# Performance work log

Measured on AMD Instinct MI355X. Metric: run time of the kernel, lower is better.

## Reference

```python
import jax, jax.numpy as jnp
import numpy as np

B, CIN, H, W = 16, 32, 256, 256
COUT, KH, KW = 32, 3, 3
NUM_EXPERTS = 8
PAD = ((1, 1), (1, 1))  # static 'same' padding for 3x3, stride 1, dilation 1


def setup_inputs() -> dict:
    key = jax.random.key(0)
    k_x, k_r, k_w, k_b = jax.random.split(key, 4)
    x = jax.random.normal(k_x, (B, CIN, H, W), dtype=jnp.float32)
    # routing weights are typically sigmoid/softmax outputs in [0,1]
    routing_weights = jax.nn.softmax(jax.random.normal(k_r, (B, NUM_EXPERTS), dtype=jnp.float32), axis=-1)
    num_params = COUT * CIN * KH * KW  # groups=1 -> in_channels//groups = CIN
    expert_weight = jax.random.normal(k_w, (NUM_EXPERTS, num_params), dtype=jnp.float32) * 0.05
    expert_bias = jax.random.normal(k_b, (NUM_EXPERTS, COUT), dtype=jnp.float32) * 0.05
    return {"x": x, "routing_weights": routing_weights,
            "expert_weight": expert_weight, "expert_bias": expert_bias}


def reference(x, routing_weights, expert_weight, expert_bias):
    b = x.shape[0]
    # Per-sample kernels: [B, num_params] -> [B, COUT, CIN, KH, KW]
    w = jnp.matmul(routing_weights, expert_weight).reshape(b, COUT, CIN, KH, KW)
    bias = jnp.matmul(routing_weights, expert_bias)  # [B, COUT]

    def conv_one(xi, wi):
        # xi: [CIN, H, W], wi: [COUT, CIN, KH, KW]
        return jax.lax.conv_general_dilated(
            xi[None], wi, window_strides=(1, 1), padding=PAD,
            dimension_numbers=("NCHW", "OIHW", "NCHW"))[0]

    out = jax.vmap(conv_one)(x, w)  # [B, COUT, H, W]
    out = out + bias[:, :, None, None]
    return out
```

## Files before the change

kernel.cpp:

```cpp
#include <hip/hip_runtime.h>

#define B_   16
#define CIN  32
#define COUT 32
#define HH   256
#define WW   256
#define NE   8
#define NTAP 9
#define KTOT (NTAP * CIN)

#define TH 8
#define TW 32
#define LROWS (TH + 2)
#define LCOLS (TW + 2)
#define PXS   40
#define NI    ((TW + 8) / 4)

typedef __attribute__((ext_vector_type(8))) short  short8;
typedef __attribute__((ext_vector_type(4))) float  floatx4;

__device__ __forceinline__ unsigned short f2bf(float f) {
    unsigned int u = __float_as_uint(f);
    u += 0x7FFFu + ((u >> 16) & 1u);
    return (unsigned short)(u >> 16);
}

__global__ __launch_bounds__(256) void prep_weights(
    const float* __restrict__ routing,
    const float* __restrict__ ew,
    const float* __restrict__ eb,
    unsigned short* __restrict__ ws_w,
    float* __restrict__ ws_b)
{
    const int b = blockIdx.x;
    const int t = threadIdx.x;
    float r[NE];
#pragma unroll
    for (int e = 0; e < NE; ++e) r[e] = routing[b * NE + e];

    for (int idx = t; idx < COUT * KTOT; idx += 256) {
        const int co  = idx / KTOT;
        const int k   = idx - co * KTOT;
        const int tap = k >> 5;
        const int ci  = k & 31;
        float acc = 0.f;
#pragma unroll
        for (int e = 0; e < NE; ++e)
            acc += r[e] * ew[e * (COUT * CIN * 9) + co * (CIN * 9) + ci * 9 + tap];
        ws_w[(b * COUT + co) * KTOT + k] = f2bf(acc);
    }
    if (t < COUT) {
        float acc = 0.f;
#pragma unroll
        for (int e = 0; e < NE; ++e) acc += r[e] * eb[e * COUT + t];
        ws_b[b * COUT + t] = acc;
    }
}

__global__ __launch_bounds__(256, 5) void condconv_mfma(
    const float* __restrict__ x,
    const unsigned short* __restrict__ wsw,
    const float* __restrict__ wsb,
    float* __restrict__ out)
{
    __shared__ __align__(16) unsigned short s_x[LROWS * LCOLS * PXS];

    const int b    = blockIdx.z;
    const int x0   = blockIdx.x * TW;
    const int y0   = blockIdx.y * TH;
    const int t    = threadIdx.x;
    const int lane = t & 63;
    const int wv   = t >> 6;
    const int ln   = lane & 15;
    const int quad = lane >> 4;

    for (int task = t; task < LROWS * NI * 4; task += 256) {
        const int cg  = task & 3;
        const int ri  = task >> 2;
        const int i   = ri % NI;
        const int row = ri / NI;
        const int gy  = y0 + row - 1;
        const int gx  = x0 + 4 * i - 4;
        floatx4 v[8];
        if (gy >= 0 && gy < HH && gx >= 0 && gx < WW) {
            const float* src = x + (((size_t)b * CIN + cg * 8) * HH + gy) * WW + gx;
#pragma unroll
            for (int u = 0; u < 8; ++u)
                v[u] = *(const floatx4*)(src + (size_t)u * HH * WW);
        } else {
#pragma unroll
            for (int u = 0; u < 8; ++u) v[u] = (floatx4){0.f, 0.f, 0.f, 0.f};
        }
#pragma unroll
        for (int j = 0; j < 4; ++j) {
            const int lcol = 4 * i + j - 3;
            if (lcol >= 0 && lcol < LCOLS) {
                short8 pk;
#pragma unroll
                for (int u = 0; u < 8; ++u) pk[u] = (short)f2bf(v[u][j]);
                *(short8*)&s_x[(row * LCOLS + lcol) * PXS + cg * 8] = pk;
            }
        }
    }

    const unsigned short* wb = wsw + (size_t)b * COUT * KTOT;
    short8 wfc0 = *(const short8*)(wb + ln * KTOT + quad * 8);
    short8 wfc1 = *(const short8*)(wb + (16 + ln) * KTOT + quad * 8);

    floatx4 acc[4][2];
#pragma unroll
    for (int tt = 0; tt < 4; ++tt)
#pragma unroll
        for (int h = 0; h < 2; ++h)
            acc[tt][h] = (floatx4){0.f, 0.f, 0.f, 0.f};

    int base[4];
#pragma unroll
    for (int tt = 0; tt < 4; ++tt)
        base[tt] = ((2 * wv + (tt >> 1)) * LCOLS + (tt & 1) * 16 + ln) * PXS + quad * 8;

    __syncthreads();

#pragma unroll 1
    for (int tap = 0; tap < NTAP; ++tap) {
        const int tn = (tap < NTAP - 1) ? tap + 1 : NTAP - 1;
        const short8 wfn0 = *(const short8*)(wb + ln * KTOT + tn * 32 + quad * 8);
        const short8 wfn1 = *(const short8*)(wb + (16 + ln) * KTOT + tn * 32 + quad * 8);
        const int dy  = tap / 3;
        const int dx  = tap - dy * 3;
        const int off = (dy * LCOLS + dx) * PXS;
#pragma unroll
        for (int tt = 0; tt < 4; ++tt) {
            const short8 pfr = *(const short8*)&s_x[base[tt] + off];
            acc[tt][0] = __builtin_amdgcn_mfma_f32_16x16x32_bf16(pfr, wfc0, acc[tt][0], 0, 0, 0);
            acc[tt][1] = __builtin_amdgcn_mfma_f32_16x16x32_bf16(pfr, wfc1, acc[tt][1], 0, 0, 0);
        }
        wfc0 = wfn0;
        wfc1 = wfn1;
    }

    float bias_v[2];
    bias_v[0] = wsb[b * COUT + ln];
    bias_v[1] = wsb[b * COUT + 16 + ln];

#pragma unroll
    for (int tt = 0; tt < 4; ++tt) {
        const int gy = y0 + 2 * wv + (tt >> 1);
        const int gx = x0 + (tt & 1) * 16 + quad * 4;
#pragma unroll
        for (int h = 0; h < 2; ++h) {
            floatx4 vo = acc[tt][h];
#pragma unroll
            for (int e = 0; e < 4; ++e) vo[e] += bias_v[h];
            const int co = h * 16 + ln;
            *(floatx4*)(out + (((size_t)b * COUT + co) * HH + gy) * WW + gx) = vo;
        }
    }
}

extern "C" void kernel_launch(void* const* d_in, const int* in_sizes, int n_in,
                              void* d_out, int out_size, void* d_ws, size_t ws_size,
                              hipStream_t stream) {
    const float* x       = (const float*)d_in[0];
    const float* routing = (const float*)d_in[1];
    const float* ew      = (const float*)d_in[2];
    const float* eb      = (const float*)d_in[3];
    float* out = (float*)d_out;

    unsigned short* ws_w = (unsigned short*)d_ws;
    float* ws_b = (float*)((char*)d_ws + (size_t)B_ * COUT * KTOT * 2);

    prep_weights<<<dim3(B_), dim3(256), 0, stream>>>(routing, ew, eb, ws_w, ws_b);

    dim3 grid(WW / TW, HH / TH, B_);
    condconv_mfma<<<grid, dim3(256), 0, stream>>>(x, ws_w, ws_b, out);
}
```

Baseline: 289.0 us.

## Stream row chunks through LDS ring buffer with register-prefetched next rows

Each block now walks 8 consecutive 8-row tiles down the image. Input rows sit in a 16-row LDS ring buffer, so the 2-row halo is reused between steps instead of being reloaded. The next 8 rows are loaded into registers while the current tile's MFMAs run. All 9 tap weight fragments and the bias are also loaded into registers once per block. The cost is more registers, fewer resident blocks (launch bounds drop from 5 to 2), fewer blocks in the grid, and two barriers per step.

```diff
diff --git a/kernel.cpp b/kernel.cpp
--- a/kernel.cpp
+++ b/kernel.cpp
@@ -9,12 +9,15 @@
 #define NTAP 9
 #define KTOT (NTAP * CIN)
 
+#define TW 32
 #define TH 8
-#define TW 32
-#define LROWS (TH + 2)
+#define NSTEP 8
+#define CHROWS (TH * NSTEP)
 #define LCOLS (TW + 2)
 #define PXS   40
-#define NI    ((TW + 8) / 4)
+#define ROWU  1536
+#define NRING 16
+#define NI    10
 
 typedef __attribute__((ext_vector_type(8))) short  short8;
 typedef __attribute__((ext_vector_type(4))) float  floatx4;
@@ -57,29 +60,39 @@
     }
 }
 
-__global__ __launch_bounds__(256, 5) void condconv_mfma(
+__global__ __launch_bounds__(256, 2) void condconv_mfma(
     const float* __restrict__ x,
     const unsigned short* __restrict__ wsw,
     const float* __restrict__ wsb,
     float* __restrict__ out)
 {
-    __shared__ __align__(16) unsigned short s_x[LROWS * LCOLS * PXS];
+    __shared__ __align__(16) unsigned short s_x[NRING * ROWU];
 
     const int b    = blockIdx.z;
     const int x0   = blockIdx.x * TW;
-    const int y0   = blockIdx.y * TH;
+    const int ych  = blockIdx.y * CHROWS;
     const int t    = threadIdx.x;
     const int lane = t & 63;
     const int wv   = t >> 6;
     const int ln   = lane & 15;
     const int quad = lane >> 4;
 
-    for (int task = t; task < LROWS * NI * 4; task += 256) {
+    const unsigned short* wb = wsw + (size_t)b * COUT * KTOT;
+    short8 wf0[NTAP], wf1[NTAP];
+#pragma unroll
+    for (int tap = 0; tap < NTAP; ++tap) {
+        wf0[tap] = *(const short8*)(wb + ln * KTOT + tap * 32 + quad * 8);
+        wf1[tap] = *(const short8*)(wb + (16 + ln) * KTOT + tap * 32 + quad * 8);
+    }
+    const float bias0 = wsb[b * COUT + ln];
+    const float bias1 = wsb[b * COUT + 16 + ln];
+
+    for (int task = t; task < 10 * NI * 4; task += 256) {
         const int cg  = task & 3;
         const int ri  = task >> 2;
         const int i   = ri % NI;
         const int row = ri / NI;
-        const int gy  = y0 + row - 1;
+        const int gy  = ych - 1 + row;
         const int gx  = x0 + 4 * i - 4;
         floatx4 v[8];
         if (gy >= 0 && gy < HH && gx >= 0 && gx < WW) {
@@ -91,6 +104,7 @@
 #pragma unroll
             for (int u = 0; u < 8; ++u) v[u] = (floatx4){0.f, 0.f, 0.f, 0.f};
         }
+        const int slot = (gy + 1) & (NRING - 1);
 #pragma unroll
         for (int j = 0; j < 4; ++j) {
             const int lcol = 4 * i + j - 3;
@@ -98,62 +112,128 @@
                 short8 pk;
 #pragma unroll
                 for (int u = 0; u < 8; ++u) pk[u] = (short)f2bf(v[u][j]);
-                *(short8*)&s_x[(row * LCOLS + lcol) * PXS + cg * 8] = pk;
-            }
-        }
-    }
-
-    const unsigned short* wb = wsw + (size_t)b * COUT * KTOT;
-    short8 wfc0 = *(const short8*)(wb + ln * KTOT + quad * 8);
-    short8 wfc1 = *(const short8*)(wb + (16 + ln) * KTOT + quad * 8);
-
-    floatx4 acc[4][2];
+                *(short8*)&s_x[slot * ROWU + lcol * PXS + cg * 8] = pk;
+            }
+        }
+    }
+
+    const int cg0  = t & 3;
+    const int ri0  = t >> 2;
+    const int i0   = ri0 % NI;
+    const int rn0  = ri0 / NI;
+    const int gx0  = x0 + 4 * i0 - 4;
+    const bool xok0 = (gx0 >= 0 && gx0 < WW);
+    const int ri1  = 64 + ri0;
+    const int i1   = ri1 % NI;
+    const int rn1  = ri1 / NI;
+    const int gx1  = x0 + 4 * i1 - 4;
+    const bool xok1 = (gx1 >= 0 && gx1 < WW);
+
+    int cpart[4];
 #pragma unroll
     for (int tt = 0; tt < 4; ++tt)
-#pragma unroll
-        for (int h = 0; h < 2; ++h)
-            acc[tt][h] = (floatx4){0.f, 0.f, 0.f, 0.f};
-
-    int base[4];
-#pragma unroll
-    for (int tt = 0; tt < 4; ++tt)
-        base[tt] = ((2 * wv + (tt >> 1)) * LCOLS + (tt & 1) * 16 + ln) * PXS + quad * 8;
+        cpart[tt] = ((tt & 1) * 16 + ln) * PXS + quad * 8;
+
+    int rb   = ych & (NRING - 1);
+    int swr0 = (ych + 10 + rn0) & (NRING - 1);
+    int swr1 = (ych + 10 + rn1) & (NRING - 1);
 
     __syncthreads();
 
 #pragma unroll 1
-    for (int tap = 0; tap < NTAP; ++tap) {
-        const int tn = (tap < NTAP - 1) ? tap + 1 : NTAP - 1;
-        const short8 wfn0 = *(const short8*)(wb + ln * KTOT + tn * 32 + quad * 8);
-        const short8 wfn1 = *(const short8*)(wb + (16 + ln) * KTOT + tn * 32 + quad * 8);
-        const int dy  = tap / 3;
-        const int dx  = tap - dy * 3;
-        const int off = (dy * LCOLS + dx) * PXS;
+    for (int k = 0; k < NSTEP; ++k) {
+        const int y0k  = ych + 8 * k;
+        const bool last = (k == NSTEP - 1);
+
+        floatx4 v0[8], v1[8];
+        if (!last) {
+            const int gyn0 = y0k + 9 + rn0;
+            if (xok0 && gyn0 < HH) {
+                const float* s0 = x + (((size_t)b * CIN + cg0 * 8) * HH + gyn0) * WW + gx0;
+#pragma unroll
+                for (int u = 0; u < 8; ++u)
+                    v0[u] = *(const floatx4*)(s0 + (size_t)u * HH * WW);
+            } else {
+#pragma unroll
+                for (int u = 0; u < 8; ++u) v0[u] = (floatx4){0.f, 0.f, 0.f, 0.f};
+            }
+            if (wv == 0) {
+                const int gyn1 = y0k + 9 + rn1;
+                if (xok1 && gyn1 < HH) {
+                    const float* s1 = x + (((size_t)b * CIN + cg0 * 8) * HH + gyn1) * WW + gx1;
+#pragma unroll
+                    for (int u = 0; u < 8; ++u)
+                        v1[u] = *(const floatx4*)(s1 + (size_t)u * HH * WW);
+                } else {
+#pragma unroll
+                    for (int u = 0; u < 8; ++u) v1[u] = (floatx4){0.f, 0.f, 0.f, 0.f};
+                }
+            }
+        }
+        __builtin_amdgcn_sched_barrier(0);
+
+        floatx4 acc[4][2];
 #pragma unroll
         for (int tt = 0; tt < 4; ++tt) {
-            const short8 pfr = *(const short8*)&s_x[base[tt] + off];
-            acc[tt][0] = __builtin_amdgcn_mfma_f32_16x16x32_bf16(pfr, wfc0, acc[tt][0], 0, 0, 0);
-            acc[tt][1] = __builtin_amdgcn_mfma_f32_16x16x32_bf16(pfr, wfc1, acc[tt][1], 0, 0, 0);
-        }
-        wfc0 = wfn0;
-        wfc1 = wfn1;
-    }
-
-    float bias_v[2];
-    bias_v[0] = wsb[b * COUT + ln];
-    bias_v[1] = wsb[b * COUT + 16 + ln];
-
-#pragma unroll
-    for (int tt = 0; tt < 4; ++tt) {
-        const int gy = y0 + 2 * wv + (tt >> 1);
-        const int gx = x0 + (tt & 1) * 16 + quad * 4;
-#pragma unroll
-        for (int h = 0; h < 2; ++h) {
-            floatx4 vo = acc[tt][h];
-#pragma unroll
-            for (int e = 0; e < 4; ++e) vo[e] += bias_v[h];
-            const int co = h * 16 + ln;
-            *(floatx4*)(out + (((size_t)b * COUT + co) * HH + gy) * WW + gx) = vo;
+            acc[tt][0] = (floatx4){0.f, 0.f, 0.f, 0.f};
+            acc[tt][1] = (floatx4){0.f, 0.f, 0.f, 0.f};
+        }
+#pragma unroll
+        for (int tap = 0; tap < NTAP; ++tap) {
+            const int dy = tap / 3;
+            const int dx = tap - dy * 3;
+            int so[2];
+#pragma unroll
+            for (int rg = 0; rg < 2; ++rg)
+                so[rg] = ((rb + 2 * wv + rg + dy) & (NRING - 1)) * ROWU + dx * PXS;
+#pragma unroll
+            for (int tt = 0; tt < 4; ++tt) {
+                const short8 pfr = *(const short8*)&s_x[so[tt >> 1] + cpart[tt]];
+                acc[tt][0] = __builtin_amdgcn_mfma_f32_16x16x32_bf16(pfr, wf0[tap], acc[tt][0], 0, 0, 0);
+                acc[tt][1] = __builtin_amdgcn_mfma_f32_16x16x32_bf16(pfr, wf1[tap], acc[tt][1], 0, 0, 0);
+            }
+        }
+
+#pragma unroll
+        for (int tt = 0; tt < 4; ++tt) {
+            const int gy = y0k + 2 * wv + (tt >> 1);
+            const int gx = x0 + (tt & 1) * 16 + quad * 4;
+            floatx4 o0 = acc[tt][0];
+            floatx4 o1 = acc[tt][1];
+#pragma unroll
+            for (int e = 0; e < 4; ++e) { o0[e] += bias0; o1[e] += bias1; }
+            *(floatx4*)(out + (((size_t)b * COUT + ln)      * HH + gy) * WW + gx) = o0;
+            *(floatx4*)(out + (((size_t)b * COUT + 16 + ln) * HH + gy) * WW + gx) = o1;
+        }
+
+        if (!last) {
+            __syncthreads();
+#pragma unroll
+            for (int j = 0; j < 4; ++j) {
+                const int lcol = 4 * i0 + j - 3;
+                if (lcol >= 0 && lcol < LCOLS) {
+                    short8 pk;
+#pragma unroll
+                    for (int u = 0; u < 8; ++u) pk[u] = (short)f2bf(v0[u][j]);
+                    *(short8*)&s_x[swr0 * ROWU + lcol * PXS + cg0 * 8] = pk;
+                }
+            }
+            if (wv == 0) {
+#pragma unroll
+                for (int j = 0; j < 4; ++j) {
+                    const int lcol = 4 * i1 + j - 3;
+                    if (lcol >= 0 && lcol < LCOLS) {
+                        short8 pk;
+#pragma unroll
+                        for (int u = 0; u < 8; ++u) pk[u] = (short)f2bf(v1[u][j]);
+                        *(short8*)&s_x[swr1 * ROWU + lcol * PXS + cg0 * 8] = pk;
+                    }
+                }
+            }
+            __syncthreads();
+            rb   = (rb + 8)   & (NRING - 1);
+            swr0 = (swr0 + 8) & (NRING - 1);
+            swr1 = (swr1 + 8) & (NRING - 1);
         }
     }
 }
@@ -172,6 +252,6 @@
 
     prep_weights<<<dim3(B_), dim3(256), 0, stream>>>(routing, ew, eb, ws_w, ws_b);
 
-    dim3 grid(WW / TW, HH / TH, B_);
+    dim3 grid(WW / TW, HH / CHROWS, B_);
     condconv_mfma<<<grid, dim3(256), 0, stream>>>(x, ws_w, ws_b, out);
 }
```

Result: slower. 296.2 us (+2.5%).

## Stream full-width row chunks through an LDS ring buffer with register-resident weights

Applied to the files above, without the earlier changes.

Replaces the small 8x32 tiles with blocks that each own a full-width strip of 16 rows. Each block keeps a 6-slot ring of bf16 input rows in LDS and prefetches the next two rows into registers while MFMAs run on the current pair. All nine tap weight fragments are loaded into registers once per block. This removes halo re-reads between neighbouring tiles and the per-tap weight loads. The cost is far fewer blocks (256 of 512 threads), higher register and LDS pressure, and two barriers per step.

```diff
diff --git a/kernel.cpp b/kernel.cpp
--- a/kernel.cpp
+++ b/kernel.cpp
@@ -9,12 +9,11 @@
 #define NTAP 9
 #define KTOT (NTAP * CIN)
 
-#define TH 8
-#define TW 32
-#define LROWS (TH + 2)
-#define LCOLS (TW + 2)
-#define PXS   40
-#define NI    ((TW + 8) / 4)
+#define CHROWS 16
+#define NSTEP  8
+#define NRING  6
+#define PXS    40
+#define SLOTU  (258 * PXS)
 
 typedef __attribute__((ext_vector_type(8))) short  short8;
 typedef __attribute__((ext_vector_type(4))) float  floatx4;
@@ -57,32 +56,49 @@
     }
 }
 
-__global__ __launch_bounds__(256, 5) void condconv_mfma(
+__global__ __launch_bounds__(512, 2) void condconv_mfma(
     const float* __restrict__ x,
     const unsigned short* __restrict__ wsw,
     const float* __restrict__ wsb,
     float* __restrict__ out)
 {
-    __shared__ __align__(16) unsigned short s_x[LROWS * LCOLS * PXS];
+    __shared__ __align__(16) unsigned short s_x[NRING * SLOTU];
 
     const int b    = blockIdx.z;
-    const int x0   = blockIdx.x * TW;
-    const int y0   = blockIdx.y * TH;
+    const int y0   = blockIdx.y * CHROWS;
     const int t    = threadIdx.x;
     const int lane = t & 63;
     const int wv   = t >> 6;
     const int ln   = lane & 15;
     const int quad = lane >> 4;
 
-    for (int task = t; task < LROWS * NI * 4; task += 256) {
+    const unsigned short* wb = wsw + (size_t)b * COUT * KTOT;
+    short8 wf0[NTAP], wf1[NTAP];
+#pragma unroll
+    for (int tap = 0; tap < NTAP; ++tap) {
+        wf0[tap] = *(const short8*)(wb + ln * KTOT + tap * 32 + quad * 8);
+        wf1[tap] = *(const short8*)(wb + (16 + ln) * KTOT + tap * 32 + quad * 8);
+    }
+    const float bias0 = wsb[b * COUT + ln];
+    const float bias1 = wsb[b * COUT + 16 + ln];
+
+    if (t < 48) {
+        const int slot = t >> 3;
+        const int rest = t & 7;
+        const int col  = (rest >> 2) ? 257 : 0;
+        const int cg   = rest & 3;
+        *(short8*)&s_x[slot * SLOTU + col * PXS + cg * 8] =
+            (short8){0, 0, 0, 0, 0, 0, 0, 0};
+    }
+
+    for (int task = t; task < 4 * 64 * 4; task += 512) {
         const int cg  = task & 3;
-        const int ri  = task >> 2;
-        const int i   = ri % NI;
-        const int row = ri / NI;
-        const int gy  = y0 + row - 1;
-        const int gx  = x0 + 4 * i - 4;
+        const int i4  = (task >> 2) & 63;
+        const int row = task >> 8;
+        const int gy  = y0 - 1 + row;
+        const int gx  = i4 * 4;
         floatx4 v[8];
-        if (gy >= 0 && gy < HH && gx >= 0 && gx < WW) {
+        if (gy >= 0 && gy < HH) {
             const float* src = x + (((size_t)b * CIN + cg * 8) * HH + gy) * WW + gx;
 #pragma unroll
             for (int u = 0; u < 8; ++u)
@@ -91,69 +107,96 @@
 #pragma unroll
             for (int u = 0; u < 8; ++u) v[u] = (floatx4){0.f, 0.f, 0.f, 0.f};
         }
+        const int slot = (gy + 1) % NRING;
 #pragma unroll
         for (int j = 0; j < 4; ++j) {
-            const int lcol = 4 * i + j - 3;
-            if (lcol >= 0 && lcol < LCOLS) {
+            short8 pk;
+#pragma unroll
+            for (int u = 0; u < 8; ++u) pk[u] = (short)f2bf(v[u][j]);
+            *(short8*)&s_x[slot * SLOTU + (gx + j + 1) * PXS + cg * 8] = pk;
+        }
+    }
+
+    const int cg0  = t & 3;
+    const int i40  = (t >> 2) & 63;
+    const int rw0  = (t >> 8) & 1;
+    const int gx0  = i40 * 4;
+
+    const int r    = wv >> 2;
+    const int xs0  = (wv & 3) * 4;
+
+    int rb = y0 % NRING;
+
+    __syncthreads();
+
+#pragma unroll 1
+    for (int k = 0; k < NSTEP; ++k) {
+        const int y0k  = y0 + 2 * k;
+        const bool last = (k == NSTEP - 1);
+        const int gyn  = y0k + 3 + rw0;
+
+        floatx4 v[8];
+        if (!last) {
+            if (gyn < HH) {
+                const float* src = x + (((size_t)b * CIN + cg0 * 8) * HH + gyn) * WW + gx0;
+#pragma unroll
+                for (int u = 0; u < 8; ++u)
+                    v[u] = *(const floatx4*)(src + (size_t)u * HH * WW);
+            } else {
+#pragma unroll
+                for (int u = 0; u < 8; ++u) v[u] = (floatx4){0.f, 0.f, 0.f, 0.f};
+            }
+        }
+        __builtin_amdgcn_sched_barrier(0);
+
+        floatx4 acc[4][2];
+#pragma unroll
+        for (int n = 0; n < 4; ++n) {
+            acc[n][0] = (floatx4){0.f, 0.f, 0.f, 0.f};
+            acc[n][1] = (floatx4){0.f, 0.f, 0.f, 0.f};
+        }
+#pragma unroll
+        for (int tap = 0; tap < NTAP; ++tap) {
+            const int dy = tap / 3;
+            const int dx = tap - dy * 3;
+            int slot = rb + r + dy;
+            slot -= (slot >= NRING) ? NRING : 0;
+            const int sb = slot * SLOTU;
+#pragma unroll
+            for (int n = 0; n < 4; ++n) {
+                const short8 pfr =
+                    *(const short8*)&s_x[sb + ((xs0 + n) * 16 + ln + dx) * PXS + quad * 8];
+                acc[n][0] = __builtin_amdgcn_mfma_f32_16x16x32_bf16(pfr, wf0[tap], acc[n][0], 0, 0, 0);
+                acc[n][1] = __builtin_amdgcn_mfma_f32_16x16x32_bf16(pfr, wf1[tap], acc[n][1], 0, 0, 0);
+            }
+        }
+
+        const int gy = y0k + r;
+#pragma unroll
+        for (int n = 0; n < 4; ++n) {
+            const int gx = (xs0 + n) * 16 + quad * 4;
+            floatx4 o0 = acc[n][0];
+            floatx4 o1 = acc[n][1];
+#pragma unroll
+            for (int e = 0; e < 4; ++e) { o0[e] += bias0; o1[e] += bias1; }
+            *(floatx4*)(out + (((size_t)b * COUT + ln)      * HH + gy) * WW + gx) = o0;
+            *(floatx4*)(out + (((size_t)b * COUT + 16 + ln) * HH + gy) * WW + gx) = o1;
+        }
+
+        if (!last) {
+            __syncthreads();
+            int slotw = rb + 4 + rw0;
+            slotw -= (slotw >= NRING) ? NRING : 0;
+#pragma unroll
+            for (int j = 0; j < 4; ++j) {
                 short8 pk;
 #pragma unroll
                 for (int u = 0; u < 8; ++u) pk[u] = (short)f2bf(v[u][j]);
-                *(short8*)&s_x[(row * LCOLS + lcol) * PXS + cg * 8] = pk;
+                *(short8*)&s_x[slotw * SLOTU + (gx0 + j + 1) * PXS + cg0 * 8] = pk;
             }
-        }
-    }
-
-    const unsigned short* wb = wsw + (size_t)b * COUT * KTOT;
-    short8 wfc0 = *(const short8*)(wb + ln * KTOT + quad * 8);
-    short8 wfc1 = *(const short8*)(wb + (16 + ln) * KTOT + quad * 8);
-
-    floatx4 acc[4][2];
-#pragma unroll
-    for (int tt = 0; tt < 4; ++tt)
-#pragma unroll
-        for (int h = 0; h < 2; ++h)
-            acc[tt][h] = (floatx4){0.f, 0.f, 0.f, 0.f};
-
-    int base[4];
-#pragma unroll
-    for (int tt = 0; tt < 4; ++tt)
-        base[tt] = ((2 * wv + (tt >> 1)) * LCOLS + (tt & 1) * 16 + ln) * PXS + quad * 8;
-
-    __syncthreads();
-
-#pragma unroll 1
-    for (int tap = 0; tap < NTAP; ++tap) {
-        const int tn = (tap < NTAP - 1) ? tap + 1 : NTAP - 1;
-        const short8 wfn0 = *(const short8*)(wb + ln * KTOT + tn * 32 + quad * 8);
-        const short8 wfn1 = *(const short8*)(wb + (16 + ln) * KTOT + tn * 32 + quad * 8);
-        const int dy  = tap / 3;
-        const int dx  = tap - dy * 3;
-        const int off = (dy * LCOLS + dx) * PXS;
-#pragma unroll
-        for (int tt = 0; tt < 4; ++tt) {
-            const short8 pfr = *(const short8*)&s_x[base[tt] + off];
-            acc[tt][0] = __builtin_amdgcn_mfma_f32_16x16x32_bf16(pfr, wfc0, acc[tt][0], 0, 0, 0);
-            acc[tt][1] = __builtin_amdgcn_mfma_f32_16x16x32_bf16(pfr, wfc1, acc[tt][1], 0, 0, 0);
-        }
-        wfc0 = wfn0;
-        wfc1 = wfn1;
-    }
-
-    float bias_v[2];
-    bias_v[0] = wsb[b * COUT + ln];
-    bias_v[1] = wsb[b * COUT + 16 + ln];
-
-#pragma unroll
-    for (int tt = 0; tt < 4; ++tt) {
-        const int gy = y0 + 2 * wv + (tt >> 1);
-        const int gx = x0 + (tt & 1) * 16 + quad * 4;
-#pragma unroll
-        for (int h = 0; h < 2; ++h) {
-            floatx4 vo = acc[tt][h];
-#pragma unroll
-            for (int e = 0; e < 4; ++e) vo[e] += bias_v[h];
-            const int co = h * 16 + ln;
-            *(floatx4*)(out + (((size_t)b * COUT + co) * HH + gy) * WW + gx) = vo;
+            __syncthreads();
+            rb += 2;
+            rb -= (rb >= NRING) ? NRING : 0;
         }
     }
 }
@@ -172,6 +215,6 @@
 
     prep_weights<<<dim3(B_), dim3(256), 0, stream>>>(routing, ew, eb, ws_w, ws_b);
 
-    dim3 grid(WW / TW, HH / TH, B_);
-    condconv_mfma<<<grid, dim3(256), 0, stream>>>(x, ws_w, ws_b, out);
-}
+    dim3 grid(1, HH / CHROWS, B_);
+    condconv_mfma<<<grid, dim3(512), 0, stream>>>(x, ws_w, ws_b, out);
+}
```

Result: no change. 287.5 us (-0.5%).
